# Kernel tuning notes

Hardware: AMD Instinct MI355X
Metric: run time of the kernel (lower is better)

## Reference

```python
import jax, jax.numpy as jnp
import numpy as np

S = 3072      # total tokens across all images
DIM = 1280    # hidden_size
H = 16        # num_heads
HD = DIM // H # head_dim = 80
NSEG = 6      # number of images (cu_seqlens has NSEG+1 entries)


def _rotate_half(x):
    x1, x2 = jnp.split(x, 2, axis=-1)
    return jnp.concatenate([-x2, x1], axis=-1)


def setup_inputs() -> dict:
    key = jax.random.key(0)
    ks = jax.random.split(key, 12)
    hidden_states = jax.random.normal(ks[0], (S, DIM), jnp.float32)
    # realistic vision rotary embedding: half-dim inv_freq, repeated to head_dim
    inv_freq = 1.0 / (10000.0 ** (jnp.arange(0, HD // 2, dtype=jnp.float32) / (HD // 2)))
    freqs = jnp.arange(S, dtype=jnp.float32)[:, None] * inv_freq[None, :]  # [S, HD/2]
    emb = jnp.concatenate([freqs, freqs], axis=-1)  # [S, HD]
    cos = jnp.cos(emb)
    sin = jnp.sin(emb)
    sc = 0.02
    wq = jax.random.normal(ks[1], (DIM, DIM), jnp.float32) * sc
    bq = jax.random.normal(ks[2], (DIM,), jnp.float32) * sc
    wk = jax.random.normal(ks[3], (DIM, DIM), jnp.float32) * sc
    bk = jax.random.normal(ks[4], (DIM,), jnp.float32) * sc
    wv = jax.random.normal(ks[5], (DIM, DIM), jnp.float32) * sc
    bv = jax.random.normal(ks[6], (DIM,), jnp.float32) * sc
    wo = jax.random.normal(ks[7], (DIM, DIM), jnp.float32) * sc
    bo = jax.random.normal(ks[8], (DIM,), jnp.float32) * sc
    cu_seqlens = (jnp.arange(NSEG + 1, dtype=jnp.int32) * (S // NSEG))  # [0,512,...,3072]
    return dict(hidden_states=hidden_states, cos=cos, sin=sin,
                wq=wq, bq=bq, wk=wk, bk=bk, wv=wv, bv=bv, wo=wo, bo=bo,
                cu_seqlens=cu_seqlens)


def reference(hidden_states, cos, sin, wq, bq, wk, bk, wv, bv, wo, bo, cu_seqlens):
    seq_length = hidden_states.shape[0]
    scaling = HD ** (-0.5)
    # QKV projections (torch Linear: x @ W.T + b)
    q = (hidden_states @ wq.T + bq).reshape(seq_length, H, HD)
    k = (hidden_states @ wk.T + bk).reshape(seq_length, H, HD)
    v = (hidden_states @ wv.T + bv).reshape(seq_length, H, HD)
    # apply_rotary_pos_emb_vision: cos/sin [S, HD] broadcast over head axis
    c = cos[:, None, :]
    s = sin[:, None, :]
    q = q * c + _rotate_half(q) * s
    k = k * c + _rotate_half(k) * s
    # block-diagonal (per-image) attention via segment mask
    seg = jnp.searchsorted(cu_seqlens[1:], jnp.arange(seq_length), side='right')
    mask = seg[:, None] == seg[None, :]  # [S, S] bool
    scores = jnp.einsum('shd,thd->hst', q, k) * scaling  # [H, S, S]
    scores = jnp.where(mask[None, :, :], scores, jnp.finfo(scores.dtype).min)
    attn = jax.nn.softmax(scores, axis=-1)
    out = jnp.einsum('hst,thd->shd', attn, v).reshape(seq_length, DIM)
    return out @ wo.T + bo
```

## Files before the change

### kernel.cpp

```cpp
#include <hip/hip_runtime.h>
#include <hip/hip_bf16.h>
#include <hip/hip_fp16.h>
#include <cstdint>
#include <cstddef>

typedef _Float16 f16;
typedef f16 f16x2 __attribute__((ext_vector_type(2)));
typedef f16 f16x4 __attribute__((ext_vector_type(4)));
typedef f16 f16x8 __attribute__((ext_vector_type(8)));
typedef float f32x4 __attribute__((ext_vector_type(4)));

#define S_LEN 3072
#define DIM 1280
#define NH 16
#define HD 80
#define SEG 512

#define MFMA16F(a, b, c) __builtin_amdgcn_mfma_f32_16x16x32_f16((a), (b), (c), 0, 0, 0)

__device__ __forceinline__ void gl2lds16(const void* g, void* l) {
    __builtin_amdgcn_global_load_lds(
        (const __attribute__((address_space(1))) unsigned int*)g,
        (__attribute__((address_space(3))) unsigned int*)l, 16, 0, 0);
}

__device__ __forceinline__ unsigned int pack2(float a, float b) {
    f16x2 t = {(f16)a, (f16)b};
    union { f16x2 v; unsigned int u; } c;
    c.v = t;
    return c.u;
}

__global__ __launch_bounds__(256) void cvt_kernel(
    const float* __restrict__ hs,
    const float* __restrict__ wq, const float* __restrict__ wk,
    const float* __restrict__ wv, const float* __restrict__ wo,
    f16* __restrict__ hs16,
    f16* __restrict__ wq16, f16* __restrict__ wk16,
    f16* __restrict__ wv16, f16* __restrict__ wo16)
{
    const int m = blockIdx.y;
    const float* src; f16* dst; int n4;
    if (m == 0)      { src = hs; dst = hs16; n4 = S_LEN * DIM / 4; }
    else if (m == 1) { src = wq; dst = wq16; n4 = DIM * DIM / 4; }
    else if (m == 2) { src = wk; dst = wk16; n4 = DIM * DIM / 4; }
    else if (m == 3) { src = wv; dst = wv16; n4 = DIM * DIM / 4; }
    else             { src = wo; dst = wo16; n4 = DIM * DIM / 4; }
    int idx = blockIdx.x * 256 + threadIdx.x;
    if (idx >= n4) return;
    f32x4 v = *(const f32x4*)(src + (size_t)idx * 4);
    f16x4 o;
#pragma unroll
    for (int e = 0; e < 4; ++e) o[e] = (f16)v[e];
    *(f16x4*)(dst + (size_t)idx * 4) = o;
}

__global__ __launch_bounds__(512, 2) void gemm_qkv192(
    const f16* __restrict__ A, const f16* __restrict__ Wb,
    const float* __restrict__ bq, const float* __restrict__ bk,
    const float* __restrict__ bv,
    f16* __restrict__ q16, f16* __restrict__ k16, f16* __restrict__ vT)
{
    const int bid = blockIdx.x;
    const int xcd = bid & 7;
    const int idx = bid >> 3;
    const int mt = xcd * 2 + idx / 15;
    const int nt = idx % 15;
    const int m0 = mt * 192;
    const int n0 = nt * 256;

    __shared__ __align__(16) f16 Abuf[2][192 * 64];
    __shared__ __align__(16) f16 Bbuf[2][256 * 64];

    const int tid = threadIdx.x;
    const int w = tid >> 6;
    const int lane = tid & 63;
    const int lane15 = lane & 15;
    const int quad = lane >> 4;
    const int wm = (w >> 2) * 96;
    const int wn = (w & 3) * 64;

    const int srow = lane >> 3;
    const int schk = (lane & 7) ^ srow;

    const int aRow = w * 24;
    const int bRow = (w & 3) * 64 + (w >> 2) * 16;

    const f16* gA = A + (size_t)(m0 + aRow + srow) * DIM + schk * 8;
    const f16* gB = Wb + (size_t)(n0 + bRow + srow) * DIM + schk * 8;

    const int x7 = lane15 & 7;
    const int cc0 = (quad ^ x7) * 8;
    const int cc1 = ((quad + 4) ^ x7) * 8;

    f32x4 acc[6][4];
#pragma unroll
    for (int i = 0; i < 6; ++i)
#pragma unroll
        for (int j = 0; j < 4; ++j)
            acc[i][j] = (f32x4){0.f, 0.f, 0.f, 0.f};

    {
        f16* lB = Bbuf[0] + bRow * 64;
        gl2lds16(gB, lB);
        gl2lds16(gB + 8 * DIM, lB + 512);
        gl2lds16(gB + 32 * DIM, lB + 2048);
        gl2lds16(gB + 40 * DIM, lB + 2560);
        f16* lA = Abuf[0] + aRow * 64;
        gl2lds16(gA, lA);
        gl2lds16(gA + 8 * DIM, lA + 512);
        gl2lds16(gA + 16 * DIM, lA + 1024);
        f16* lB1 = Bbuf[1] + bRow * 64;
        gl2lds16(gB + 64, lB1);
        gl2lds16(gB + 8 * DIM + 64, lB1 + 512);
        gl2lds16(gB + 32 * DIM + 64, lB1 + 2048);
        gl2lds16(gB + 40 * DIM + 64, lB1 + 2560);
        f16* lA1 = Abuf[1] + aRow * 64;
        gl2lds16(gA + 64, lA1);
        gl2lds16(gA + 8 * DIM + 64, lA1 + 512);
        gl2lds16(gA + 16 * DIM + 64, lA1 + 1024);
    }
    asm volatile("s_waitcnt vmcnt(7)" ::: "memory");
    __builtin_amdgcn_s_barrier();

    f16x8 a0[3][2], a1[3][2], b01[2][2], b23[2][2];
#pragma unroll
    for (int i = 0; i < 3; ++i) {
        const f16* rp = Abuf[0] + (wm + i * 16 + lane15) * 64;
        a0[i][0] = *(const f16x8*)(rp + cc0);
        a0[i][1] = *(const f16x8*)(rp + cc1);
    }
#pragma unroll
    for (int j = 0; j < 2; ++j) {
        const f16* rp = Bbuf[0] + (wn + j * 16 + lane15) * 64;
        b01[j][0] = *(const f16x8*)(rp + cc0);
        b01[j][1] = *(const f16x8*)(rp + cc1);
    }

    for (int kt = 0; kt < 20; ++kt) {
        const int s = kt & 1;
        const int sn = s ^ 1;
        const int k2 = (kt + 2 < 20) ? kt + 2 : 19;
        const f16* As = Abuf[s];
        const f16* Bsl = Bbuf[s];
        const f16* Asn = Abuf[sn];
        const f16* Bsn = Bbuf[sn];
        const f16* gA2 = gA + k2 * 64;
        const f16* gB2 = gB + k2 * 64;

        __builtin_amdgcn_s_barrier();
        asm volatile("s_waitcnt lgkmcnt(0)" ::: "memory");
        __builtin_amdgcn_sched_barrier(0);
        __builtin_amdgcn_s_setprio(1);
#pragma unroll
        for (int i = 0; i < 3; ++i)
#pragma unroll
            for (int j = 0; j < 2; ++j) {
                acc[i][j] = MFMA16F(a0[i][0], b01[j][0], acc[i][j]);
                acc[i][j] = MFMA16F(a0[i][1], b01[j][1], acc[i][j]);
            }
        __builtin_amdgcn_s_setprio(0);
        __builtin_amdgcn_sched_barrier(0);
#pragma unroll
        for (int j = 0; j < 2; ++j) {
            const f16* rp = Bsl + (wn + 32 + j * 16 + lane15) * 64;
            b23[j][0] = *(const f16x8*)(rp + cc0);
            b23[j][1] = *(const f16x8*)(rp + cc1);
        }

        __builtin_amdgcn_s_barrier();
        asm volatile("s_waitcnt lgkmcnt(0)" ::: "memory");
        __builtin_amdgcn_sched_barrier(0);
        __builtin_amdgcn_s_setprio(1);
#pragma unroll
        for (int i = 0; i < 3; ++i)
#pragma unroll
            for (int j = 0; j < 2; ++j) {
                acc[i][j + 2] = MFMA16F(a0[i][0], b23[j][0], acc[i][j + 2]);
                acc[i][j + 2] = MFMA16F(a0[i][1], b23[j][1], acc[i][j + 2]);
            }
        __builtin_amdgcn_s_setprio(0);
        __builtin_amdgcn_sched_barrier(0);
#pragma unroll
        for (int i = 0; i < 3; ++i) {
            const f16* rp = As + (wm + 48 + i * 16 + lane15) * 64;
            a1[i][0] = *(const f16x8*)(rp + cc0);
            a1[i][1] = *(const f16x8*)(rp + cc1);
        }
        {
            f16* lB = Bbuf[s] + bRow * 64;
            gl2lds16(gB2, lB);
            gl2lds16(gB2 + 8 * DIM, lB + 512);
            gl2lds16(gB2 + 32 * DIM, lB + 2048);
            gl2lds16(gB2 + 40 * DIM, lB + 2560);
        }
        asm volatile("s_waitcnt vmcnt(4)" ::: "memory");

        __builtin_amdgcn_s_barrier();
        asm volatile("s_waitcnt lgkmcnt(0)" ::: "memory");
        __builtin_amdgcn_sched_barrier(0);
        __builtin_amdgcn_s_setprio(1);
#pragma unroll
        for (int i = 0; i < 3; ++i)
#pragma unroll
            for (int j = 0; j < 2; ++j) {
                acc[i + 3][j + 2] = MFMA16F(a1[i][0], b23[j][0], acc[i + 3][j + 2]);
                acc[i + 3][j + 2] = MFMA16F(a1[i][1], b23[j][1], acc[i + 3][j + 2]);
            }
        __builtin_amdgcn_s_setprio(0);
        __builtin_amdgcn_sched_barrier(0);
#pragma unroll
        for (int i = 0; i < 3; ++i) {
            const f16* rp = Asn + (wm + i * 16 + lane15) * 64;
            a0[i][0] = *(const f16x8*)(rp + cc0);
            a0[i][1] = *(const f16x8*)(rp + cc1);
        }
        {
            f16* lA = Abuf[s] + aRow * 64;
            gl2lds16(gA2, lA);
            gl2lds16(gA2 + 8 * DIM, lA + 512);
            gl2lds16(gA2 + 16 * DIM, lA + 1024);
        }

        __builtin_amdgcn_s_barrier();
        asm volatile("s_waitcnt lgkmcnt(0)" ::: "memory");
        __builtin_amdgcn_sched_barrier(0);
        __builtin_amdgcn_s_setprio(1);
#pragma unroll
        for (int i = 0; i < 3; ++i)
#pragma unroll
            for (int j = 0; j < 2; ++j) {
                acc[i + 3][j] = MFMA16F(a1[i][0], b01[j][0], acc[i + 3][j]);
                acc[i + 3][j] = MFMA16F(a1[i][1], b01[j][1], acc[i + 3][j]);
            }
        __builtin_amdgcn_s_setprio(0);
        __builtin_amdgcn_sched_barrier(0);
#pragma unroll
        for (int j = 0; j < 2; ++j) {
            const f16* rp = Bsn + (wn + j * 16 + lane15) * 64;
            b01[j][0] = *(const f16x8*)(rp + cc0);
            b01[j][1] = *(const f16x8*)(rp + cc1);
        }
    }
    asm volatile("s_waitcnt vmcnt(0) lgkmcnt(0)" ::: "memory");

    const int sel = nt / 5;
    const int nc0 = (nt % 5) * 256 + wn;
    const float* bias = (sel == 0) ? bq : (sel == 1) ? bk : bv;
    float bvv[4];
#pragma unroll
    for (int j = 0; j < 4; ++j) bvv[j] = bias[nc0 + j * 16 + lane15];

    if (sel < 2) {
        f16* O = sel ? k16 : q16;
#pragma unroll
        for (int i = 0; i < 6; ++i)
#pragma unroll
            for (int j = 0; j < 4; ++j)
#pragma unroll
                for (int r = 0; r < 4; ++r) {
                    int row = m0 + wm + i * 16 + quad * 4 + r;
                    O[(size_t)row * DIM + nc0 + j * 16 + lane15] =
                        (f16)(acc[i][j][r] + bvv[j]);
                }
    } else {
#pragma unroll
        for (int i = 0; i < 6; ++i)
#pragma unroll
            for (int j = 0; j < 4; ++j) {
                f16x4 ov;
#pragma unroll
                for (int r = 0; r < 4; ++r) ov[r] = (f16)(acc[i][j][r] + bvv[j]);
                int row = m0 + wm + i * 16 + quad * 4;
                int col = nc0 + j * 16 + lane15;
                *(f16x4*)(vT + (size_t)col * S_LEN + row) = ov;
            }
    }
}

__global__ __launch_bounds__(256) void gemm_out_kernel(
    const f16* __restrict__ A, const f16* __restrict__ W,
    const float* __restrict__ bias, float* __restrict__ OF)
{
    const int f = blockIdx.x;
    const int xcd = f & 7;
    const int idx = f >> 3;
    const int xt = xcd * 6 + idx % 6;
    const int yt = idx / 6;

    __shared__ __align__(16) f16 As[64 * 32];
    __shared__ __align__(16) f16 Bs[128 * 32];

    const int tid = threadIdx.x;
    const int lane = tid & 63;
    const int lane15 = tid & 15;
    const int quad = lane >> 4;
    const int w = tid >> 6;
    const int wn = w * 32;
    const int m0 = xt * 64;
    const int n0 = yt * 128;

    const int srA = w * 16 + (lane >> 2);
    const int srB = w * 32 + (lane >> 2);
    const int scol = (lane & 3) * 8;
    const f16* gA0 = A + (size_t)(m0 + srA) * DIM + scol;
    const f16* gB0 = W + (size_t)(n0 + srB) * DIM + scol;
    const f16* gB1 = W + (size_t)(n0 + srB + 16) * DIM + scol;
    f16* lA0 = As + (w * 16) * 32;
    f16* lB0 = Bs + (w * 32) * 32;
    f16* lB1 = Bs + (w * 32 + 16) * 32;

    f32x4 acc[4][2];
#pragma unroll
    for (int i = 0; i < 4; ++i)
#pragma unroll
        for (int j = 0; j < 2; ++j)
            acc[i][j] = (f32x4){0.f, 0.f, 0.f, 0.f};

    for (int kt = 0; kt < DIM / 32; ++kt) {
        __syncthreads();
        gl2lds16(gA0 + kt * 32, lA0);
        gl2lds16(gB0 + kt * 32, lB0);
        gl2lds16(gB1 + kt * 32, lB1);
        __syncthreads();

        f16x8 fa[4], fb[2];
#pragma unroll
        for (int i = 0; i < 4; ++i)
            fa[i] = *(const f16x8*)(As + (i * 16 + lane15) * 32 + quad * 8);
#pragma unroll
        for (int j = 0; j < 2; ++j)
            fb[j] = *(const f16x8*)(Bs + (wn + j * 16 + lane15) * 32 + quad * 8);
#pragma unroll
        for (int i = 0; i < 4; ++i)
#pragma unroll
            for (int j = 0; j < 2; ++j)
                acc[i][j] = MFMA16F(fa[i], fb[j], acc[i][j]);
    }

    float bvv[2];
#pragma unroll
    for (int j = 0; j < 2; ++j)
        bvv[j] = bias[n0 + wn + j * 16 + lane15];

#pragma unroll
    for (int i = 0; i < 4; ++i)
#pragma unroll
        for (int j = 0; j < 2; ++j)
#pragma unroll
            for (int r = 0; r < 4; ++r) {
                int row = m0 + i * 16 + quad * 4 + r;
                int col = n0 + wn + j * 16 + lane15;
                OF[(size_t)row * DIM + col] = acc[i][j][r] + bvv[j];
            }
}

__global__ __launch_bounds__(256) void rope_kernel(
    f16* __restrict__ qb, f16* __restrict__ kb,
    const float* __restrict__ cosb, const float* __restrict__ sinb)
{
    int idx = blockIdx.x * 256 + threadIdx.x;
    int c = idx % 5;
    int t = idx / 5;
    int h = t & 15; t >>= 4;
    int s = t % S_LEN;
    int which = t / S_LEN;
    f16* buf = which ? kb : qb;
    float scale = which ? 1.0f : 0.11180339887498948f;
    int j = c * 8;
    f32x4 ca = *(const f32x4*)(cosb + s * HD + j);
    f32x4 cb = *(const f32x4*)(cosb + s * HD + j + 4);
    f32x4 sna = *(const f32x4*)(sinb + s * HD + j);
    f32x4 snb = *(const f32x4*)(sinb + s * HD + j + 4);
    size_t base = (size_t)s * DIM + h * HD + j;
    f16x8 x1 = *(f16x8*)(buf + base);
    f16x8 x2 = *(f16x8*)(buf + base + 40);
    f16x8 o1, o2;
#pragma unroll
    for (int e = 0; e < 8; ++e) {
        float ce = (e < 4) ? ca[e] : cb[e - 4];
        float se = (e < 4) ? sna[e] : snb[e - 4];
        float a = (float)x1[e], b = (float)x2[e];
        o1[e] = (f16)((a * ce - b * se) * scale);
        o2[e] = (f16)((b * ce + a * se) * scale);
    }
    *(f16x8*)(buf + base) = o1;
    *(f16x8*)(buf + base + 40) = o2;
}

__global__ __launch_bounds__(256) void attn_kernel(
    const f16* __restrict__ q, const f16* __restrict__ k,
    const f16* __restrict__ vT, f16* __restrict__ o)
{
    const int h = blockIdx.x;
    const int g = blockIdx.y;
    const int qc = blockIdx.z;
    const int tid = threadIdx.x;
    const int lane15 = tid & 15;
    const int quad = (tid & 63) >> 4;
    const int w = tid >> 6;
    const int qbase = g * SEG + qc * 64;
    const int qrow = qbase + w * 16 + lane15;

    __shared__ __align__(16) f16 Ks[128 * 88];
    __shared__ __align__(16) f16 Vt[80 * 128];

    f16x8 zf;
#pragma unroll
    for (int e = 0; e < 8; ++e) zf[e] = (f16)0.0f;

    f16x8 fq[3];
#pragma unroll
    for (int kc = 0; kc < 3; ++kc) {
        if (kc == 2 && quad >= 2) fq[kc] = zf;
        else fq[kc] = *(const f16x8*)(q + (size_t)qrow * DIM + h * HD + kc * 32 + quad * 8);
    }

    float m_run = -1e30f, l_run = 0.f;
    f32x4 Oa[5];
#pragma unroll
    for (int dt = 0; dt < 5; ++dt) Oa[dt] = (f32x4){0.f, 0.f, 0.f, 0.f};

    for (int kt = 0; kt < 4; ++kt) {
        __syncthreads();
        const int kb = g * SEG + kt * 128;
#pragma unroll
        for (int c = tid; c < 1280; c += 256) {
            int r = c / 10;
            int c8 = (c - r * 10) * 8;
            *(f16x8*)(Ks + r * 88 + c8) =
                *(const f16x8*)(k + (size_t)(kb + r) * DIM + h * HD + c8);
        }
#pragma unroll
        for (int c = tid; c < 1280; c += 256) {
            int d = c >> 4;
            int sc = c & 15;
            *(f16x8*)(Vt + d * 128 + (sc ^ (d & 7)) * 8) =
                *(const f16x8*)(vT + (size_t)(h * HD + d) * S_LEN + kb + sc * 8);
        }
        __syncthreads();

        f32x4 sa[8];
#pragma unroll
        for (int nt = 0; nt < 8; ++nt) sa[nt] = (f32x4){0.f, 0.f, 0.f, 0.f};
#pragma unroll
        for (int kc = 0; kc < 3; ++kc) {
#pragma unroll
            for (int nt = 0; nt < 8; ++nt) {
                f16x8 fk;
                if (kc == 2 && quad >= 2) fk = zf;
                else fk = *(const f16x8*)(Ks + (nt * 16 + lane15) * 88 + kc * 32 + quad * 8);
                sa[nt] = MFMA16F(fk, fq[kc], sa[nt]);
            }
        }

        float mt = -1e30f;
#pragma unroll
        for (int nt = 0; nt < 8; ++nt)
#pragma unroll
            for (int r = 0; r < 4; ++r) mt = fmaxf(mt, sa[nt][r]);
        mt = fmaxf(mt, __shfl_xor(mt, 16, 64));
        mt = fmaxf(mt, __shfl_xor(mt, 32, 64));

        float mn = fmaxf(m_run, mt);
        float alpha = __expf(m_run - mn);
        m_run = mn;
        float lt = 0.f;
        unsigned int pp[8][2];
#pragma unroll
        for (int nt = 0; nt < 8; ++nt) {
            float p0 = __expf(sa[nt][0] - mn);
            float p1 = __expf(sa[nt][1] - mn);
            float p2 = __expf(sa[nt][2] - mn);
            float p3 = __expf(sa[nt][3] - mn);
            lt += (p0 + p1) + (p2 + p3);
            pp[nt][0] = pack2(p0, p1);
            pp[nt][1] = pack2(p2, p3);
        }
        lt += __shfl_xor(lt, 16, 64);
        lt += __shfl_xor(lt, 32, 64);
        l_run = l_run * alpha + lt;

#pragma unroll
        for (int dt = 0; dt < 5; ++dt)
#pragma unroll
            for (int r = 0; r < 4; ++r) Oa[dt][r] *= alpha;

        const int srcA = ((quad & 1) * 2) * 16 + lane15;
        const int srcB = srcA + 16;
        const bool hi = quad >= 2;
#pragma unroll
        for (int kc2 = 0; kc2 < 4; ++kc2) {
            unsigned int e0 = __shfl((int)pp[2 * kc2][0], srcA, 64);
            unsigned int e1 = __shfl((int)pp[2 * kc2][1], srcA, 64);
            unsigned int e2 = __shfl((int)pp[2 * kc2][0], srcB, 64);
            unsigned int e3 = __shfl((int)pp[2 * kc2][1], srcB, 64);
            unsigned int o0 = __shfl((int)pp[2 * kc2 + 1][0], srcA, 64);
            unsigned int o1 = __shfl((int)pp[2 * kc2 + 1][1], srcA, 64);
            unsigned int o2 = __shfl((int)pp[2 * kc2 + 1][0], srcB, 64);
            unsigned int o3 = __shfl((int)pp[2 * kc2 + 1][1], srcB, 64);
            union { unsigned int u[4]; f16x8 v; } fp;
            fp.u[0] = hi ? o0 : e0;
            fp.u[1] = hi ? o1 : e1;
            fp.u[2] = hi ? o2 : e2;
            fp.u[3] = hi ? o3 : e3;
#pragma unroll
            for (int dt = 0; dt < 5; ++dt) {
                int drow = dt * 16 + lane15;
                int slot = (kc2 * 4 + quad) ^ (drow & 7);
                f16x8 fv = *(const f16x8*)(Vt + drow * 128 + slot * 8);
                Oa[dt] = MFMA16F(fv, fp.v, Oa[dt]);
            }
        }
    }

    float inv = 1.0f / l_run;
#pragma unroll
    for (int dt = 0; dt < 5; ++dt) {
        f16x4 ov;
#pragma unroll
        for (int r = 0; r < 4; ++r) ov[r] = (f16)(Oa[dt][r] * inv);
        *(f16x4*)(o + (size_t)qrow * DIM + h * HD + dt * 16 + quad * 4) = ov;
    }
}

extern "C" void kernel_launch(void* const* d_in, const int* in_sizes, int n_in,
                              void* d_out, int out_size, void* d_ws, size_t ws_size,
                              hipStream_t stream)
{
    const float* hs   = (const float*)d_in[0];
    const float* cosb = (const float*)d_in[1];
    const float* sinb = (const float*)d_in[2];
    const float* wq   = (const float*)d_in[3];
    const float* bq   = (const float*)d_in[4];
    const float* wk   = (const float*)d_in[5];
    const float* bk   = (const float*)d_in[6];
    const float* wv   = (const float*)d_in[7];
    const float* bv   = (const float*)d_in[8];
    const float* wo   = (const float*)d_in[9];
    const float* bo   = (const float*)d_in[10];

    const size_t SD = (size_t)S_LEN * DIM;
    const size_t WW = (size_t)DIM * DIM;
    f16* hs16 = (f16*)d_ws;
    f16* wq16 = hs16 + SD;
    f16* wk16 = wq16 + WW;
    f16* wv16 = wk16 + WW;
    f16* wo16 = wv16 + WW;
    f16* q16  = wo16 + WW;
    f16* k16  = q16 + SD;
    f16* vT16 = k16 + SD;
    f16* ao16 = vT16 + SD;
    float* outb = (float*)d_out;

    cvt_kernel<<<dim3(S_LEN * DIM / 4 / 256, 5), 256, 0, stream>>>(
        hs, wq, wk, wv, wo, hs16, wq16, wk16, wv16, wo16);
    gemm_qkv192<<<240, 512, 0, stream>>>(
        hs16, wq16, bq, bk, bv, q16, k16, vT16);
    rope_kernel<<<1920, 256, 0, stream>>>(q16, k16, cosb, sinb);
    attn_kernel<<<dim3(NH, 6, 8), 256, 0, stream>>>(q16, k16, vT16, ao16);
    gemm_out_kernel<<<480, 256, 0, stream>>>(ao16, wo16, bo, outb);
}
```

Before: 215.0 us.

## Prefetch next K/V tile into registers and swizzle K LDS layout

The attention kernel now loads the next 128-key K and V^T tile from global memory into registers while the current tile's MFMAs run, then writes them to LDS at the top of the next iteration. K in shared memory is re-laid out as chunk-major with an XOR swizzle instead of padded rows, which aims to cut bank conflicts. A launch bound of 4 blocks per CU is added. In exchange, register pressure rises from holding ten f16x8 prefetch registers, which may cause spills under the occupancy cap.

Result: slower. 232.9 us (+8.3%).

```diff
diff --git a/kernel.cpp b/kernel.cpp
--- a/kernel.cpp
+++ b/kernel.cpp
@@ -388,7 +388,7 @@
     *(f16x8*)(buf + base + 40) = o2;
 }
 
-__global__ __launch_bounds__(256) void attn_kernel(
+__global__ __launch_bounds__(256, 4) void attn_kernel(
     const f16* __restrict__ q, const f16* __restrict__ k,
     const f16* __restrict__ vT, f16* __restrict__ o)
 {
@@ -402,12 +402,20 @@
     const int qbase = g * SEG + qc * 64;
     const int qrow = qbase + w * 16 + lane15;
 
-    __shared__ __align__(16) f16 Ks[128 * 88];
+    __shared__ __align__(16) f16 Ks2[10 * 128 * 8];
     __shared__ __align__(16) f16 Vt[80 * 128];
 
     f16x8 zf;
 #pragma unroll
     for (int e = 0; e < 8; ++e) zf[e] = (f16)0.0f;
+
+    int kr[5], kch[5];
+#pragma unroll
+    for (int i = 0; i < 5; ++i) {
+        int c = tid + 256 * i;
+        kr[i] = c / 10;
+        kch[i] = c - kr[i] * 10;
+    }
 
     f16x8 fq[3];
 #pragma unroll
@@ -416,6 +424,20 @@
         else fq[kc] = *(const f16x8*)(q + (size_t)qrow * DIM + h * HD + kc * 32 + quad * 8);
     }
 
+    f16x8 kreg[5], vreg[5];
+    {
+        const int kb = g * SEG;
+#pragma unroll
+        for (int i = 0; i < 5; ++i)
+            kreg[i] = *(const f16x8*)(k + (size_t)(kb + kr[i]) * DIM + h * HD + kch[i] * 8);
+#pragma unroll
+        for (int i = 0; i < 5; ++i) {
+            int c = tid + 256 * i;
+            int d = c >> 4, sc = c & 15;
+            vreg[i] = *(const f16x8*)(vT + (size_t)(h * HD + d) * S_LEN + kb + sc * 8);
+        }
+    }
+
     float m_run = -1e30f, l_run = 0.f;
     f32x4 Oa[5];
 #pragma unroll
@@ -423,22 +445,31 @@
 
     for (int kt = 0; kt < 4; ++kt) {
         __syncthreads();
-        const int kb = g * SEG + kt * 128;
-#pragma unroll
-        for (int c = tid; c < 1280; c += 256) {
-            int r = c / 10;
-            int c8 = (c - r * 10) * 8;
-            *(f16x8*)(Ks + r * 88 + c8) =
-                *(const f16x8*)(k + (size_t)(kb + r) * DIM + h * HD + c8);
-        }
-#pragma unroll
-        for (int c = tid; c < 1280; c += 256) {
-            int d = c >> 4;
-            int sc = c & 15;
-            *(f16x8*)(Vt + d * 128 + (sc ^ (d & 7)) * 8) =
-                *(const f16x8*)(vT + (size_t)(h * HD + d) * S_LEN + kb + sc * 8);
+#pragma unroll
+        for (int i = 0; i < 5; ++i) {
+            int rr = kr[i] ^ (kch[i] & 7);
+            *(f16x8*)(Ks2 + kch[i] * 1024 + rr * 8) = kreg[i];
+        }
+#pragma unroll
+        for (int i = 0; i < 5; ++i) {
+            int c = tid + 256 * i;
+            int d = c >> 4, sc = c & 15;
+            *(f16x8*)(Vt + d * 128 + (sc ^ (d & 7)) * 8) = vreg[i];
         }
         __syncthreads();
+
+        if (kt < 3) {
+            const int kb = g * SEG + (kt + 1) * 128;
+#pragma unroll
+            for (int i = 0; i < 5; ++i)
+                kreg[i] = *(const f16x8*)(k + (size_t)(kb + kr[i]) * DIM + h * HD + kch[i] * 8);
+#pragma unroll
+            for (int i = 0; i < 5; ++i) {
+                int c = tid + 256 * i;
+                int d = c >> 4, sc = c & 15;
+                vreg[i] = *(const f16x8*)(vT + (size_t)(h * HD + d) * S_LEN + kb + sc * 8);
+            }
+        }
 
         f32x4 sa[8];
 #pragma unroll
@@ -449,7 +480,11 @@
             for (int nt = 0; nt < 8; ++nt) {
                 f16x8 fk;
                 if (kc == 2 && quad >= 2) fk = zf;
-                else fk = *(const f16x8*)(Ks + (nt * 16 + lane15) * 88 + kc * 32 + quad * 8);
+                else {
+                    int ch = kc * 4 + quad;
+                    int rr = (nt * 16 + lane15) ^ (ch & 7);
+                    fk = *(const f16x8*)(Ks2 + ch * 1024 + rr * 8);
+                }
                 sa[nt] = MFMA16F(fk, fq[kc], sa[nt]);
             }
         }
```
